# Kernel optimization log

Hardware: AMD Instinct MI355X
Metric: run time of the kernel (lower is better)

## Reference

```python
import jax, jax.numpy as jnp
import numpy as np

B, H, W = 4, 128, 128
D_MODEL = 256
N_LAYERS = 4
N_STATE = 64


def _s4d_kernel(log_dt, logA_re, A_im, C_re, C_im, L):
    """S4D (diagonal SSM) convolution kernel of length L. Shapes: log_dt (d,), others (d,N). Returns (d, L)."""
    dt = jnp.exp(log_dt)                       # (d,)
    A = -jnp.exp(logA_re) + 1j * A_im          # (d,N) complex, Re<0 for stability
    C = C_re + 1j * C_im                       # (d,N)
    dtA = dt[:, None] * A                      # (d,N)
    # ZOH-style input matrix folded into C (S4D-Lin):  C * (exp(dt*A)-1)/A
    CB = C * (jnp.exp(dtA) - 1.0) / A          # (d,N)
    pows = jnp.exp(dtA[:, :, None] * jnp.arange(L, dtype=jnp.float32))  # (d,N,L)
    K = jnp.einsum('dn,dnl->dl', CB, pows)     # (d,L) complex
    return 2.0 * K.real


def _layernorm(x, w, b, eps=1e-5):
    mu = jnp.mean(x, axis=-1, keepdims=True)
    var = jnp.mean(jnp.square(x - mu), axis=-1, keepdims=True)
    return (x - mu) * jax.lax.rsqrt(var + eps) * w + b


def setup_inputs() -> dict:
    key = jax.random.key(0)
    ks = jax.random.split(key, 16)
    d, L, N = D_MODEL, N_LAYERS, N_STATE
    x = jax.random.normal(ks[0], (B, H, W, 1), dtype=jnp.float32)
    grid = jax.random.uniform(ks[1], (B, H, W, 1), dtype=jnp.float32)
    W_enc = jax.random.normal(ks[2], (2, d), dtype=jnp.float32) / np.sqrt(2.0)
    b_enc = jnp.zeros((d,), jnp.float32)
    # per-layer, per-axis (axis 0 = H-kernel, axis 1 = W-kernel) SSM params
    log_dt = jax.random.uniform(ks[3], (L, 2, d), jnp.float32,
                                minval=float(np.log(1e-3)), maxval=float(np.log(1e-1)))
    logA_re = jnp.full((L, 2, d, N), float(np.log(0.5)), jnp.float32)
    A_im = jnp.broadcast_to(np.pi * jnp.arange(N, dtype=jnp.float32), (L, 2, d, N)).copy()
    C_re = jax.random.normal(ks[4], (L, 2, d, N), jnp.float32) * float(0.5 ** 0.5)
    C_im = jax.random.normal(ks[5], (L, 2, d, N), jnp.float32) * float(0.5 ** 0.5)
    Dskip = jax.random.normal(ks[6], (L, d), jnp.float32)
    W_out = jax.random.normal(ks[7], (L, d, 2 * d), jnp.float32) / np.sqrt(d)
    b_out = jnp.zeros((L, 2 * d), jnp.float32)
    ln_w = jnp.ones((L, d), jnp.float32)
    ln_b = jnp.zeros((L, d), jnp.float32)
    W_dec = jax.random.normal(ks[8], (d, 1), jnp.float32) / np.sqrt(d)
    b_dec = jnp.zeros((1,), jnp.float32)
    return dict(x=x, grid=grid, W_enc=W_enc, b_enc=b_enc, log_dt=log_dt,
                logA_re=logA_re, A_im=A_im, C_re=C_re, C_im=C_im, Dskip=Dskip,
                W_out=W_out, b_out=b_out, ln_w=ln_w, ln_b=ln_b, W_dec=W_dec, b_dec=b_dec)


def reference(x, grid, W_enc, b_enc, log_dt, logA_re, A_im, C_re, C_im,
              Dskip, W_out, b_out, ln_w, ln_b, W_dec, b_dec):
    # encoder: concat grid, project to d_model  -> (B,H,W,d)
    h = jnp.concatenate([x, grid], axis=-1) @ W_enc + b_enc
    n_fft = (2 * H, 2 * W)
    for i in range(N_LAYERS):
        z = h
        # separable 2D S4ND kernel: outer product of per-axis S4D kernels
        kh = _s4d_kernel(log_dt[i, 0], logA_re[i, 0], A_im[i, 0], C_re[i, 0], C_im[i, 0], H)  # (d,H)
        kw = _s4d_kernel(log_dt[i, 1], logA_re[i, 1], A_im[i, 1], C_re[i, 1], C_im[i, 1], W)  # (d,W)
        K2 = kh[:, :, None] * kw[:, None, :]                     # (d,H,W)
        u = jnp.transpose(z, (0, 3, 1, 2))                       # (B,d,H,W)
        yf = jnp.fft.rfft2(u, s=n_fft) * jnp.fft.rfft2(K2, s=n_fft)
        y = jnp.fft.irfft2(yf, s=n_fft)[..., :H, :W]             # causal 2D conv via zero-pad FFT
        y = y + u * Dskip[i][:, None, None]                      # skip connection D*u
        y = jnp.transpose(y, (0, 2, 3, 1))                       # back to (B,H,W,d)
        y = jax.nn.gelu(y)
        y = y @ W_out[i] + b_out[i]                              # (B,H,W,2d)
        a, g = jnp.split(y, 2, axis=-1)
        y = a * jax.nn.sigmoid(g)                                # GLU output linear
        h = y + h                                                # residual (dropout=0, eval)
        h = _layernorm(h, ln_w[i], ln_b[i])                      # post-norm (prenorm=False)
    return h @ W_dec + b_dec                                     # (B,H,W,1)
```

## Files before the change

### kernel.cpp

```cpp
#include <hip/hip_runtime.h>
#include <math.h>

#define DM 256
#define NS 64
#define SP 128

typedef __attribute__((ext_vector_type(8))) short bf16x8;
typedef __attribute__((ext_vector_type(4))) float f32x4;

__device__ __forceinline__ float gelu_f(float x) {
    float x3 = x * x * x;
    return 0.5f * x * (1.0f + tanhf(0.7978845608028654f * (x + 0.044715f * x3)));
}
__device__ __forceinline__ float sigmoid_f(float x) {
    return 1.0f / (1.0f + expf(-x));
}
__device__ __forceinline__ unsigned short f2bf(float f) {
    unsigned u = __float_as_uint(f);
    u += 0x7fff + ((u >> 16) & 1);
    return (unsigned short)(u >> 16);
}
__device__ __forceinline__ float bf2f(unsigned short b) {
    return __uint_as_float(((unsigned)b) << 16);
}

__global__ __launch_bounds__(128) void gen_k_kernel(
        const float* __restrict__ log_dt, const float* __restrict__ logA_re,
        const float* __restrict__ A_im,   const float* __restrict__ C_re,
        const float* __restrict__ C_im,   float* __restrict__ Kd) {
    int blk = blockIdx.x;
    int d  = blk & (DM - 1);
    int la = blk >> 8;
    int q  = threadIdx.x;
    __shared__ float s_cbr[NS], s_cbi[NS], s_dr[NS], s_di[NS];
    int pbase = (la * DM + d) * NS;
    float dt = expf(log_dt[la * DM + d]);
    if (q < NS) {
        int n = q;
        float ar = -expf(logA_re[pbase + n]);
        float ai = A_im[pbase + n];
        float dr = dt * ar, di = dt * ai;
        float er = expf(dr);
        float sn, cs;
        sincosf(di, &sn, &cs);
        float nr = er * cs - 1.0f, ni = er * sn;
        float inv = 1.0f / (ar * ar + ai * ai);
        float br = (nr * ar + ni * ai) * inv;
        float bi = (ni * ar - nr * ai) * inv;
        float cr = C_re[pbase + n], ci = C_im[pbase + n];
        s_cbr[n] = cr * br - ci * bi;
        s_cbi[n] = cr * bi + ci * br;
        s_dr[n] = dr;
        s_di[n] = di;
    }
    __syncthreads();
    float fq = (float)q;
    float acc = 0.0f;
    for (int n = 0; n < NS; ++n) {
        float pr = expf(s_dr[n] * fq);
        float sn, cs;
        sincosf(s_di[n] * fq, &sn, &cs);
        acc += s_cbr[n] * (pr * cs) - s_cbi[n] * (pr * sn);
    }
    Kd[((size_t)la * DM + d) * SP + q] = 2.0f * acc;
}

__global__ __launch_bounds__(256) void toep_kernel(
        const float* __restrict__ Kd, unsigned short* __restrict__ Tp, int l) {
    int blk = blockIdx.x;
    int axis = blk >> 8, d = blk & 255;
    int la = l * 2 + axis;
    __shared__ float kt[SP];
    if (threadIdx.x < SP) kt[threadIdx.x] = Kd[((size_t)la * DM + d) * SP + threadIdx.x];
    __syncthreads();
    size_t bse = ((size_t)axis * DM + d) * 16384;
    for (int e = threadIdx.x; e < 16384; e += 256) {
        int i = e >> 7, j = e & 127;
        Tp[bse + e] = (j <= i) ? f2bf(kt[i - j]) : (unsigned short)0;
    }
}

__global__ __launch_bounds__(256) void prep_b_kernel(
        const float* __restrict__ Wo, unsigned short* __restrict__ Bt) {
    int idx = blockIdx.x * 256 + threadIdx.x;
    int l = idx >> 17, rem = idx & 131071, n = rem >> 8, k = rem & 255;
    Bt[idx] = f2bf(Wo[(size_t)l * 131072 + k * 512 + n]);
}

__global__ __launch_bounds__(256) void encode_kernel(
        const float* __restrict__ x, const float* __restrict__ g,
        const float* __restrict__ W_enc, const float* __restrict__ b_enc,
        unsigned short* __restrict__ h) {
    int total = 4 * SP * SP * 128;
    for (int idx = blockIdx.x * blockDim.x + threadIdx.x; idx < total;
         idx += gridDim.x * blockDim.x) {
        int c = (idx & 127) * 2;
        int pos = idx >> 7;
        float xv = x[pos], gv = g[pos];
        float v0 = xv * W_enc[c] + gv * W_enc[DM + c] + b_enc[c];
        float v1 = xv * W_enc[c + 1] + gv * W_enc[DM + c + 1] + b_enc[c + 1];
        unsigned o = (unsigned)f2bf(v0) | ((unsigned)f2bf(v1) << 16);
        *(unsigned*)(h + (size_t)pos * DM + c) = o;
    }
}

template <int FUSE>
__global__ __launch_bounds__(256) void transpose_kernel(
        const unsigned short* __restrict__ in, unsigned short* __restrict__ out,
        int Ci, int Ri, int ctmask, int ctshift,
        const unsigned short* __restrict__ hres, const float* __restrict__ Dsk) {
    __shared__ unsigned tile[64][65];
    int bid = blockIdx.x;
    int rt = bid >> ctshift, ct = bid & ctmask;
    int r0 = rt << 6, c0 = ct << 6;
    int tid = threadIdx.x;
    #pragma unroll
    for (int rep = 0; rep < 2; ++rep) {
        int e = rep * 256 + tid;
        int p = e >> 3, cc = e & 7;
        uint4 v = *(const uint4*)(in + (size_t)(r0 + p) * Ci + c0 + cc * 8);
        const unsigned short* pv = (const unsigned short*)&v;
        #pragma unroll
        for (int q = 0; q < 8; ++q) tile[p][cc * 8 + q] = pv[q];
    }
    __syncthreads();
    #pragma unroll
    for (int rep = 0; rep < 2; ++rep) {
        int e = rep * 256 + tid;
        int cc = e >> 3, pc = e & 7;
        unsigned short tmp[8];
        #pragma unroll
        for (int q = 0; q < 8; ++q) tmp[q] = (unsigned short)tile[pc * 8 + q][cc];
        size_t oaddr = (size_t)(c0 + cc) * Ri + r0 + pc * 8;
        if (FUSE) {
            int d0 = r0 + pc * 8;
            uint4 hv = *(const uint4*)(hres + oaddr);
            const unsigned short* hvp = (const unsigned short*)&hv;
            float4 dk0 = *(const float4*)(Dsk + d0);
            float4 dk1 = *(const float4*)(Dsk + d0 + 4);
            #pragma unroll
            for (int q = 0; q < 8; ++q) {
                float dk = (q < 4) ? (&dk0.x)[q] : (&dk1.x)[q - 4];
                float z = fmaf(bf2f(hvp[q]), dk, bf2f(tmp[q]));
                tmp[q] = f2bf(gelu_f(z));
            }
        }
        *(uint4*)(out + oaddr) = *(const uint4*)tmp;
    }
}

__global__ __launch_bounds__(512, 4) void conv_kernel(
        const unsigned short* __restrict__ hc, const unsigned short* __restrict__ Tp,
        unsigned short* __restrict__ Zc) {
    __shared__ unsigned short Tile[128][128];
    __shared__ unsigned short TpL[128][128];
    int bid = blockIdx.x;
    int work = (bid & 7) * 128 + (bid >> 3);
    int d = work >> 2, b = work & 3;
    int tid = threadIdx.x;
    int lane = tid & 63, wv = tid >> 6;
    int lc = lane & 15, g = lane >> 4;

    const unsigned short* TpW = Tp + (size_t)(DM + d) * 16384;
    const unsigned short* TpH = Tp + (size_t)d * 16384;

    {
        const uint4* srcU = (const uint4*)(hc + ((size_t)d * 4 + b) * 16384);
        const uint4* srcT = (const uint4*)TpW;
        #pragma unroll
        for (int it = 0; it < 4; ++it) {
            int e = it * 512 + tid;
            int r = e >> 4, wc = e & 15;
            *(uint4*)&Tile[r][((wc ^ (r & 7)) << 3)] = srcU[e];
            *(uint4*)&TpL[r][((wc ^ (r & 7)) << 3)] = srcT[e];
        }
    }
    __syncthreads();

    f32x4 acc[8];
    #pragma unroll
    for (int ni = 0; ni < 8; ++ni) acc[ni] = (f32x4){0.f, 0.f, 0.f, 0.f};
    #pragma unroll
    for (int kk = 0; kk < 4; ++kk) {
        int hh = wv * 16 + lc;
        bf16x8 a = *(const bf16x8*)&Tile[hh][(((kk * 4 + g) ^ (hh & 7)) << 3)];
        #pragma unroll
        for (int ni = 0; ni < 8; ++ni) {
            int n = ni * 16 + lc;
            bf16x8 bf = *(const bf16x8*)&TpL[n][(((kk * 4 + g) ^ (n & 7)) << 3)];
            acc[ni] = __builtin_amdgcn_mfma_f32_16x16x32_bf16(a, bf, acc[ni], 0, 0, 0);
        }
    }
    __syncthreads();

    {
        int hh0 = wv * 16 + g * 4;
        #pragma unroll
        for (int ni = 0; ni < 8; ++ni) {
            int w = ni * 16 + lc;
            ushort4 p;
            p.x = f2bf(acc[ni][0]); p.y = f2bf(acc[ni][1]);
            p.z = f2bf(acc[ni][2]); p.w = f2bf(acc[ni][3]);
            *(ushort4*)&Tile[w][((((hh0 >> 3) ^ (w & 7)) << 3) | (hh0 & 7))] = p;
        }
        const uint4* srcT = (const uint4*)TpH;
        #pragma unroll
        for (int it = 0; it < 4; ++it) {
            int e = it * 512 + tid;
            int r = e >> 4, wc = e & 15;
            *(uint4*)&TpL[r][((wc ^ (r & 7)) << 3)] = srcT[e];
        }
    }
    __syncthreads();

    #pragma unroll
    for (int ni = 0; ni < 8; ++ni) acc[ni] = (f32x4){0.f, 0.f, 0.f, 0.f};
    #pragma unroll
    for (int kk = 0; kk < 4; ++kk) {
        int w = wv * 16 + lc;
        bf16x8 a = *(const bf16x8*)&Tile[w][(((kk * 4 + g) ^ (w & 7)) << 3)];
        #pragma unroll
        for (int ni = 0; ni < 8; ++ni) {
            int n = ni * 16 + lc;
            bf16x8 bf = *(const bf16x8*)&TpL[n][(((kk * 4 + g) ^ (n & 7)) << 3)];
            acc[ni] = __builtin_amdgcn_mfma_f32_16x16x32_bf16(a, bf, acc[ni], 0, 0, 0);
        }
    }
    __syncthreads();

    {
        int w0 = wv * 16 + g * 4;
        #pragma unroll
        for (int ni = 0; ni < 8; ++ni) {
            int hh = ni * 16 + lc;
            ushort4 p;
            p.x = f2bf(acc[ni][0]); p.y = f2bf(acc[ni][1]);
            p.z = f2bf(acc[ni][2]); p.w = f2bf(acc[ni][3]);
            *(ushort4*)&Tile[hh][((((w0 >> 3) ^ (hh & 7)) << 3) | (w0 & 7))] = p;
        }
    }
    __syncthreads();
    {
        uint4* dst = (uint4*)(Zc + ((size_t)d * 4 + b) * 16384);
        #pragma unroll
        for (int it = 0; it < 4; ++it) {
            int e = it * 512 + tid;
            int r = e >> 4, wc = e & 15;
            dst[e] = *(const uint4*)&Tile[r][((wc ^ (r & 7)) << 3)];
        }
    }
}

__global__ __launch_bounds__(512, 4) void glu_kernel(
        const unsigned short* __restrict__ Ab, const unsigned short* __restrict__ Bt,
        const unsigned short* __restrict__ h, unsigned short* __restrict__ hp,
        const float* __restrict__ bo) {
    __shared__ unsigned short Ba[64][256];
    __shared__ unsigned short Bg[64][256];
    int tid = threadIdx.x;
    int lane = tid & 63, wv = tid >> 6;
    int lc = lane & 15, g = lane >> 4;
    int m0 = blockIdx.x * 128;
    int mrow = m0 + wv * 16 + lc;

    bf16x8 af[8];
    #pragma unroll
    for (int kk = 0; kk < 8; ++kk)
        af[kk] = *(const bf16x8*)(Ab + (size_t)mrow * DM + kk * 32 + g * 8);

    #pragma unroll
    for (int qp = 0; qp < 4; ++qp) {
        {
            const uint4* srcA = (const uint4*)(Bt + (size_t)(qp * 64) * DM);
            const uint4* srcG = (const uint4*)(Bt + (size_t)(256 + qp * 64) * DM);
            #pragma unroll
            for (int it = 0; it < 4; ++it) {
                int e = it * 512 + tid;
                int r = e >> 5, wc = e & 31;
                *(uint4*)&Ba[r][((wc ^ (r & 7)) << 3)] = srcA[e];
                *(uint4*)&Bg[r][((wc ^ (r & 7)) << 3)] = srcG[e];
            }
        }
        __syncthreads();

        f32x4 aa[4], ag[4];
        #pragma unroll
        for (int ni = 0; ni < 4; ++ni) {
            aa[ni] = (f32x4){0.f, 0.f, 0.f, 0.f};
            ag[ni] = (f32x4){0.f, 0.f, 0.f, 0.f};
        }
        #pragma unroll
        for (int kk = 0; kk < 8; ++kk) {
            #pragma unroll
            for (int ni = 0; ni < 4; ++ni) {
                int r = ni * 16 + lc;
                int ch = (((kk * 4 + g) ^ (r & 7)) << 3);
                bf16x8 bfa = *(const bf16x8*)&Ba[r][ch];
                bf16x8 bfg = *(const bf16x8*)&Bg[r][ch];
                aa[ni] = __builtin_amdgcn_mfma_f32_16x16x32_bf16(bfa, af[kk], aa[ni], 0, 0, 0);
                ag[ni] = __builtin_amdgcn_mfma_f32_16x16x32_bf16(bfg, af[kk], ag[ni], 0, 0, 0);
            }
        }

        #pragma unroll
        for (int ni = 0; ni < 4; ++ni) {
            int ca = qp * 64 + ni * 16 + g * 4;
            float4 bav = *(const float4*)(bo + ca);
            float4 bgv = *(const float4*)(bo + 256 + ca);
            size_t pbase = (size_t)mrow * DM + ca;
            uint2 hv = *(const uint2*)(h + pbase);
            float hr[4];
            hr[0] = __uint_as_float(hv.x << 16);
            hr[1] = __uint_as_float(hv.x & 0xffff0000u);
            hr[2] = __uint_as_float(hv.y << 16);
            hr[3] = __uint_as_float(hv.y & 0xffff0000u);
            float o[4];
            #pragma unroll
            for (int reg = 0; reg < 4; ++reg)
                o[reg] = (aa[ni][reg] + (&bav.x)[reg]) * sigmoid_f(ag[ni][reg] + (&bgv.x)[reg]) + hr[reg];
            uint2 ov;
            ov.x = (unsigned)f2bf(o[0]) | ((unsigned)f2bf(o[1]) << 16);
            ov.y = (unsigned)f2bf(o[2]) | ((unsigned)f2bf(o[3]) << 16);
            *(uint2*)(hp + pbase) = ov;
        }
        __syncthreads();
    }
}

__global__ __launch_bounds__(256) void ln_kernel(
        const unsigned short* __restrict__ hp, unsigned short* __restrict__ h,
        const float* __restrict__ lnw, const float* __restrict__ lnb) {
    int pos = blockIdx.x * 4 + (threadIdx.x >> 6);
    int lane = threadIdx.x & 63;
    size_t base = (size_t)pos * DM + lane * 4;
    uint2 hv = *(const uint2*)(hp + base);
    float v[4];
    v[0] = __uint_as_float(hv.x << 16);
    v[1] = __uint_as_float(hv.x & 0xffff0000u);
    v[2] = __uint_as_float(hv.y << 16);
    v[3] = __uint_as_float(hv.y & 0xffff0000u);
    float s1 = v[0] + v[1] + v[2] + v[3];
    float s2 = v[0] * v[0] + v[1] * v[1] + v[2] * v[2] + v[3] * v[3];
    #pragma unroll
    for (int off = 1; off < 64; off <<= 1) {
        s1 += __shfl_xor(s1, off);
        s2 += __shfl_xor(s2, off);
    }
    float mean = s1 * (1.0f / 256.0f);
    float var = s2 * (1.0f / 256.0f) - mean * mean;
    float inv = rsqrtf(var + 1e-5f);
    float4 w4 = *(const float4*)(lnw + lane * 4);
    float4 b4 = *(const float4*)(lnb + lane * 4);
    float o0 = (v[0] - mean) * inv * w4.x + b4.x;
    float o1 = (v[1] - mean) * inv * w4.y + b4.y;
    float o2 = (v[2] - mean) * inv * w4.z + b4.z;
    float o3 = (v[3] - mean) * inv * w4.w + b4.w;
    uint2 ov;
    ov.x = (unsigned)f2bf(o0) | ((unsigned)f2bf(o1) << 16);
    ov.y = (unsigned)f2bf(o2) | ((unsigned)f2bf(o3) << 16);
    *(uint2*)(h + base) = ov;
}

__global__ __launch_bounds__(256) void decode_kernel(
        const unsigned short* __restrict__ h, const float* __restrict__ Wd,
        const float* __restrict__ bd, float* __restrict__ out) {
    int pos = blockIdx.x * 4 + (threadIdx.x >> 6);
    int lane = threadIdx.x & 63;
    float s = 0.0f;
    #pragma unroll
    for (int j = 0; j < 4; ++j) {
        int d = j * 64 + lane;
        s += bf2f(h[(size_t)pos * DM + d]) * Wd[d];
    }
    #pragma unroll
    for (int off = 32; off > 0; off >>= 1) s += __shfl_down(s, off);
    if (lane == 0) out[pos] = s + bd[0];
}

extern "C" void kernel_launch(void* const* d_in, const int* in_sizes, int n_in,
                              void* d_out, int out_size, void* d_ws, size_t ws_size,
                              hipStream_t stream) {
    const float* x       = (const float*)d_in[0];
    const float* grid    = (const float*)d_in[1];
    const float* W_enc   = (const float*)d_in[2];
    const float* b_enc   = (const float*)d_in[3];
    const float* log_dt  = (const float*)d_in[4];
    const float* logA_re = (const float*)d_in[5];
    const float* A_im    = (const float*)d_in[6];
    const float* C_re    = (const float*)d_in[7];
    const float* C_im    = (const float*)d_in[8];
    const float* Dskip   = (const float*)d_in[9];
    const float* W_out   = (const float*)d_in[10];
    const float* b_out   = (const float*)d_in[11];
    const float* ln_w    = (const float*)d_in[12];
    const float* ln_b    = (const float*)d_in[13];
    const float* W_dec   = (const float*)d_in[14];
    const float* b_dec   = (const float*)d_in[15];

    char* base = (char*)d_ws;
    float*          Kd  = (float*)base;
    unsigned short* Bt  = (unsigned short*)(base + 1048576);
    unsigned short* hP  = (unsigned short*)(base + 2097152);
    unsigned short* R1  = (unsigned short*)(base + 35651584);
    unsigned short* R2  = (unsigned short*)(base + 69206016);
    unsigned short* Tp  = (unsigned short*)(base + 102760448);

    gen_k_kernel<<<dim3(8 * DM), dim3(128), 0, stream>>>(log_dt, logA_re, A_im,
                                                         C_re, C_im, Kd);
    prep_b_kernel<<<dim3(2048), dim3(256), 0, stream>>>(W_out, Bt);
    encode_kernel<<<dim3(2048), dim3(256), 0, stream>>>(x, grid, W_enc, b_enc, hP);

    for (int l = 0; l < 4; ++l) {
        toep_kernel<<<dim3(512), dim3(256), 0, stream>>>(Kd, Tp, l);
        transpose_kernel<0><<<dim3(4096), dim3(256), 0, stream>>>(
            hP, R1, 256, 65536, 3, 2, (const unsigned short*)nullptr, (const float*)nullptr);
        conv_kernel<<<dim3(1024), dim3(512), 0, stream>>>(R1, Tp, R2);
        transpose_kernel<1><<<dim3(4096), dim3(256), 0, stream>>>(
            R2, R1, 65536, 256, 1023, 10, hP, Dskip + (size_t)l * DM);
        glu_kernel<<<dim3(512), dim3(512), 0, stream>>>(R1,
            Bt + (size_t)l * 131072, hP, R2, b_out + (size_t)l * 512);
        ln_kernel<<<dim3(16384), dim3(256), 0, stream>>>(R2, hP,
            ln_w + (size_t)l * DM, ln_b + (size_t)l * DM);
    }

    decode_kernel<<<dim3(16384), dim3(256), 0, stream>>>(hP, W_dec, b_dec,
                                                         (float*)d_out);
}
```

Before: 512.0 us.

## Fuse transposes, skip-GELU, GLU and LayerNorm into one kernel per layer

Replaces the per-layer chain of transpose, transpose+skip+GELU, GLU and LayerNorm kernels with one glu_ln kernel. It reads the channel-major conv output and residual directly, transposes through LDS, and computes GELU, the GEMM with GLU, and the row LayerNorm. It then writes the result in both position-major and channel-major layouts, so the next layer's input transpose is no longer needed. This cuts several full-tensor HBM round trips and launches per layer, at the cost of about 100KB of LDS per block, which lowers occupancy to 2 blocks per CU, plus strided channel-major loads and stores.

Measured after the change: 602.0 us. 1.18x slower.

```diff
diff --git a/kernel.cpp b/kernel.cpp
--- a/kernel.cpp
+++ b/kernel.cpp
@@ -104,11 +104,9 @@
     }
 }
 
-template <int FUSE>
 __global__ __launch_bounds__(256) void transpose_kernel(
         const unsigned short* __restrict__ in, unsigned short* __restrict__ out,
-        int Ci, int Ri, int ctmask, int ctshift,
-        const unsigned short* __restrict__ hres, const float* __restrict__ Dsk) {
+        int Ci, int Ri, int ctmask, int ctshift) {
     __shared__ unsigned tile[64][65];
     int bid = blockIdx.x;
     int rt = bid >> ctshift, ct = bid & ctmask;
@@ -131,21 +129,7 @@
         unsigned short tmp[8];
         #pragma unroll
         for (int q = 0; q < 8; ++q) tmp[q] = (unsigned short)tile[pc * 8 + q][cc];
-        size_t oaddr = (size_t)(c0 + cc) * Ri + r0 + pc * 8;
-        if (FUSE) {
-            int d0 = r0 + pc * 8;
-            uint4 hv = *(const uint4*)(hres + oaddr);
-            const unsigned short* hvp = (const unsigned short*)&hv;
-            float4 dk0 = *(const float4*)(Dsk + d0);
-            float4 dk1 = *(const float4*)(Dsk + d0 + 4);
-            #pragma unroll
-            for (int q = 0; q < 8; ++q) {
-                float dk = (q < 4) ? (&dk0.x)[q] : (&dk1.x)[q - 4];
-                float z = fmaf(bf2f(hvp[q]), dk, bf2f(tmp[q]));
-                tmp[q] = f2bf(gelu_f(z));
-            }
-        }
-        *(uint4*)(out + oaddr) = *(const uint4*)tmp;
+        *(uint4*)(out + (size_t)(c0 + cc) * Ri + r0 + pc * 8) = *(const uint4*)tmp;
     }
 }
 
@@ -251,23 +235,49 @@
     }
 }
 
-__global__ __launch_bounds__(512, 4) void glu_kernel(
-        const unsigned short* __restrict__ Ab, const unsigned short* __restrict__ Bt,
-        const unsigned short* __restrict__ h, unsigned short* __restrict__ hp,
-        const float* __restrict__ bo) {
+__global__ __launch_bounds__(512, 2) void glu_ln_kernel(
+        const unsigned short* __restrict__ Zc, const unsigned short* __restrict__ Bt,
+        unsigned short* __restrict__ hP, unsigned short* __restrict__ hc,
+        const float* __restrict__ Dsk, const float* __restrict__ bo,
+        const float* __restrict__ lnw, const float* __restrict__ lnb) {
     __shared__ unsigned short Ba[64][256];
     __shared__ unsigned short Bg[64][256];
+    __shared__ unsigned short Ot[128][256];
+    __shared__ float rs[128][2];
     int tid = threadIdx.x;
     int lane = tid & 63, wv = tid >> 6;
     int lc = lane & 15, g = lane >> 4;
     int m0 = blockIdx.x * 128;
-    int mrow = m0 + wv * 16 + lc;
+    int arow = wv * 16 + lc;
+    int mrow = m0 + arow;
+
+    #pragma unroll
+    for (int it = 0; it < 8; ++it) {
+        int e = it * 512 + tid;
+        int ch = e >> 4, pck = e & 15;
+        uint4 zv = *(const uint4*)(Zc + (size_t)ch * 65536 + m0 + pck * 8);
+        uint4 hv = *(const uint4*)(hc + (size_t)ch * 65536 + m0 + pck * 8);
+        float dk = Dsk[ch];
+        const unsigned short* zp = (const unsigned short*)&zv;
+        const unsigned short* hq = (const unsigned short*)&hv;
+        #pragma unroll
+        for (int p = 0; p < 8; ++p) {
+            int pos = pck * 8 + p;
+            float a = gelu_f(fmaf(bf2f(hq[p]), dk, bf2f(zp[p])));
+            Ot[pos][(((ch >> 3) ^ (pos & 7)) << 3) | (ch & 7)] = f2bf(a);
+        }
+    }
+    __syncthreads();
 
     bf16x8 af[8];
     #pragma unroll
-    for (int kk = 0; kk < 8; ++kk)
-        af[kk] = *(const bf16x8*)(Ab + (size_t)mrow * DM + kk * 32 + g * 8);
-
+    for (int kk = 0; kk < 8; ++kk) {
+        int ck = (kk * 4 + g) ^ (arow & 7);
+        af[kk] = *(const bf16x8*)&Ot[arow][ck << 3];
+    }
+    __syncthreads();
+
+    float s1 = 0.f, s2 = 0.f;
     #pragma unroll
     for (int qp = 0; qp < 4; ++qp) {
         {
@@ -307,8 +317,7 @@
             int ca = qp * 64 + ni * 16 + g * 4;
             float4 bav = *(const float4*)(bo + ca);
             float4 bgv = *(const float4*)(bo + 256 + ca);
-            size_t pbase = (size_t)mrow * DM + ca;
-            uint2 hv = *(const uint2*)(h + pbase);
+            uint2 hv = *(const uint2*)(hP + (size_t)mrow * DM + ca);
             float hr[4];
             hr[0] = __uint_as_float(hv.x << 16);
             hr[1] = __uint_as_float(hv.x & 0xffff0000u);
@@ -316,49 +325,61 @@
             hr[3] = __uint_as_float(hv.y & 0xffff0000u);
             float o[4];
             #pragma unroll
-            for (int reg = 0; reg < 4; ++reg)
+            for (int reg = 0; reg < 4; ++reg) {
                 o[reg] = (aa[ni][reg] + (&bav.x)[reg]) * sigmoid_f(ag[ni][reg] + (&bgv.x)[reg]) + hr[reg];
-            uint2 ov;
-            ov.x = (unsigned)f2bf(o[0]) | ((unsigned)f2bf(o[1]) << 16);
-            ov.y = (unsigned)f2bf(o[2]) | ((unsigned)f2bf(o[3]) << 16);
-            *(uint2*)(hp + pbase) = ov;
+                s1 += o[reg];
+                s2 += o[reg] * o[reg];
+            }
+            unsigned* wp = (unsigned*)&Ot[arow][((((ca >> 3) ^ (arow & 7)) << 3) | (ca & 7))];
+            wp[0] = (unsigned)f2bf(o[0]) | ((unsigned)f2bf(o[1]) << 16);
+            wp[1] = (unsigned)f2bf(o[2]) | ((unsigned)f2bf(o[3]) << 16);
         }
         __syncthreads();
     }
-}
-
-__global__ __launch_bounds__(256) void ln_kernel(
-        const unsigned short* __restrict__ hp, unsigned short* __restrict__ h,
-        const float* __restrict__ lnw, const float* __restrict__ lnb) {
-    int pos = blockIdx.x * 4 + (threadIdx.x >> 6);
-    int lane = threadIdx.x & 63;
-    size_t base = (size_t)pos * DM + lane * 4;
-    uint2 hv = *(const uint2*)(hp + base);
-    float v[4];
-    v[0] = __uint_as_float(hv.x << 16);
-    v[1] = __uint_as_float(hv.x & 0xffff0000u);
-    v[2] = __uint_as_float(hv.y << 16);
-    v[3] = __uint_as_float(hv.y & 0xffff0000u);
-    float s1 = v[0] + v[1] + v[2] + v[3];
-    float s2 = v[0] * v[0] + v[1] * v[1] + v[2] * v[2] + v[3] * v[3];
-    #pragma unroll
-    for (int off = 1; off < 64; off <<= 1) {
-        s1 += __shfl_xor(s1, off);
-        s2 += __shfl_xor(s2, off);
-    }
+
+    s1 += __shfl_xor(s1, 16); s2 += __shfl_xor(s2, 16);
+    s1 += __shfl_xor(s1, 32); s2 += __shfl_xor(s2, 32);
     float mean = s1 * (1.0f / 256.0f);
     float var = s2 * (1.0f / 256.0f) - mean * mean;
     float inv = rsqrtf(var + 1e-5f);
-    float4 w4 = *(const float4*)(lnw + lane * 4);
-    float4 b4 = *(const float4*)(lnb + lane * 4);
-    float o0 = (v[0] - mean) * inv * w4.x + b4.x;
-    float o1 = (v[1] - mean) * inv * w4.y + b4.y;
-    float o2 = (v[2] - mean) * inv * w4.z + b4.z;
-    float o3 = (v[3] - mean) * inv * w4.w + b4.w;
-    uint2 ov;
-    ov.x = (unsigned)f2bf(o0) | ((unsigned)f2bf(o1) << 16);
-    ov.y = (unsigned)f2bf(o2) | ((unsigned)f2bf(o3) << 16);
-    *(uint2*)(h + base) = ov;
+    if (g == 0) { rs[arow][0] = mean; rs[arow][1] = inv; }
+    __syncthreads();
+
+    #pragma unroll
+    for (int it = 0; it < 8; ++it) {
+        int e = it * 512 + tid;
+        int row = e >> 5, ck = e & 31;
+        int c0 = ck * 8;
+        uint4 v = *(const uint4*)&Ot[row][((ck ^ (row & 7)) << 3)];
+        const unsigned short* vp = (const unsigned short*)&v;
+        float mn = rs[row][0], iv = rs[row][1];
+        float4 w0 = *(const float4*)(lnw + c0);
+        float4 w1 = *(const float4*)(lnw + c0 + 4);
+        float4 b0 = *(const float4*)(lnb + c0);
+        float4 b1 = *(const float4*)(lnb + c0 + 4);
+        unsigned short tmp[8];
+        #pragma unroll
+        for (int q = 0; q < 8; ++q) {
+            float lw = (q < 4) ? (&w0.x)[q] : (&w1.x)[q - 4];
+            float lb = (q < 4) ? (&b0.x)[q] : (&b1.x)[q - 4];
+            tmp[q] = f2bf((bf2f(vp[q]) - mn) * iv * lw + lb);
+        }
+        *(uint4*)(hP + (size_t)(m0 + row) * DM + c0) = *(const uint4*)tmp;
+    }
+    #pragma unroll
+    for (int it = 0; it < 8; ++it) {
+        int e = it * 512 + tid;
+        int ch = e >> 4, pck = e & 15;
+        float lw = lnw[ch], lb = lnb[ch];
+        unsigned short tmp[8];
+        #pragma unroll
+        for (int p = 0; p < 8; ++p) {
+            int pos = pck * 8 + p;
+            float v = bf2f(Ot[pos][(((ch >> 3) ^ (pos & 7)) << 3) | (ch & 7)]);
+            tmp[p] = f2bf((v - rs[pos][0]) * rs[pos][1] * lw + lb);
+        }
+        *(uint4*)(hc + (size_t)ch * 65536 + m0 + pck * 8) = *(const uint4*)tmp;
+    }
 }
 
 __global__ __launch_bounds__(256) void decode_kernel(
@@ -401,25 +422,22 @@
     float*          Kd  = (float*)base;
     unsigned short* Bt  = (unsigned short*)(base + 1048576);
     unsigned short* hP  = (unsigned short*)(base + 2097152);
-    unsigned short* R1  = (unsigned short*)(base + 35651584);
-    unsigned short* R2  = (unsigned short*)(base + 69206016);
+    unsigned short* HC  = (unsigned short*)(base + 35651584);
+    unsigned short* ZC  = (unsigned short*)(base + 69206016);
     unsigned short* Tp  = (unsigned short*)(base + 102760448);
 
     gen_k_kernel<<<dim3(8 * DM), dim3(128), 0, stream>>>(log_dt, logA_re, A_im,
                                                          C_re, C_im, Kd);
     prep_b_kernel<<<dim3(2048), dim3(256), 0, stream>>>(W_out, Bt);
     encode_kernel<<<dim3(2048), dim3(256), 0, stream>>>(x, grid, W_enc, b_enc, hP);
+    transpose_kernel<<<dim3(4096), dim3(256), 0, stream>>>(hP, HC, 256, 65536, 3, 2);
 
     for (int l = 0; l < 4; ++l) {
         toep_kernel<<<dim3(512), dim3(256), 0, stream>>>(Kd, Tp, l);
-        transpose_kernel<0><<<dim3(4096), dim3(256), 0, stream>>>(
-            hP, R1, 256, 65536, 3, 2, (const unsigned short*)nullptr, (const float*)nullptr);
-        conv_kernel<<<dim3(1024), dim3(512), 0, stream>>>(R1, Tp, R2);
-        transpose_kernel<1><<<dim3(4096), dim3(256), 0, stream>>>(
-            R2, R1, 65536, 256, 1023, 10, hP, Dskip + (size_t)l * DM);
-        glu_kernel<<<dim3(512), dim3(512), 0, stream>>>(R1,
-            Bt + (size_t)l * 131072, hP, R2, b_out + (size_t)l * 512);
-        ln_kernel<<<dim3(16384), dim3(256), 0, stream>>>(R2, hP,
+        conv_kernel<<<dim3(1024), dim3(512), 0, stream>>>(HC, Tp, ZC);
+        glu_ln_kernel<<<dim3(512), dim3(512), 0, stream>>>(ZC,
+            Bt + (size_t)l * 131072, hP, HC,
+            Dskip + (size_t)l * DM, b_out + (size_t)l * 512,
             ln_w + (size_t)l * DM, ln_b + (size_t)l * DM);
     }
 
```

## Fuse layernorm with channel-major transpose and restructure GLU tiling per output quarter

Applied to the files above, without the earlier changes.

The per-layer channel-major transpose moves into a new layernorm kernel. That kernel normalizes rows in place and also writes the transposed copy that the next layer's conv reads, so one full pass over the activations per layer is removed. Only the initial transpose stays outside the loop. The GLU kernel is restructured so each block loads one 64-column slice of the weights once and reuses it across 512 rows. It now writes its output in place into h instead of into a separate buffer. The risk is an in-place hazard: GLU reads h as the residual and writes h in the same place, which is fine only while each element is read before it is written by the same thread.

Result: slower. 533.3 us (+4.2%).

```diff
diff --git a/kernel.cpp b/kernel.cpp
--- a/kernel.cpp
+++ b/kernel.cpp
@@ -253,35 +253,35 @@
 
 __global__ __launch_bounds__(512, 4) void glu_kernel(
         const unsigned short* __restrict__ Ab, const unsigned short* __restrict__ Bt,
-        const unsigned short* __restrict__ h, unsigned short* __restrict__ hp,
-        const float* __restrict__ bo) {
+        unsigned short* __restrict__ h, const float* __restrict__ bo) {
     __shared__ unsigned short Ba[64][256];
     __shared__ unsigned short Bg[64][256];
     int tid = threadIdx.x;
     int lane = tid & 63, wv = tid >> 6;
     int lc = lane & 15, g = lane >> 4;
-    int m0 = blockIdx.x * 128;
-    int mrow = m0 + wv * 16 + lc;
-
-    bf16x8 af[8];
-    #pragma unroll
-    for (int kk = 0; kk < 8; ++kk)
-        af[kk] = *(const bf16x8*)(Ab + (size_t)mrow * DM + kk * 32 + g * 8);
-
-    #pragma unroll
-    for (int qp = 0; qp < 4; ++qp) {
-        {
-            const uint4* srcA = (const uint4*)(Bt + (size_t)(qp * 64) * DM);
-            const uint4* srcG = (const uint4*)(Bt + (size_t)(256 + qp * 64) * DM);
-            #pragma unroll
-            for (int it = 0; it < 4; ++it) {
-                int e = it * 512 + tid;
-                int r = e >> 5, wc = e & 31;
-                *(uint4*)&Ba[r][((wc ^ (r & 7)) << 3)] = srcA[e];
-                *(uint4*)&Bg[r][((wc ^ (r & 7)) << 3)] = srcG[e];
-            }
-        }
-        __syncthreads();
+    int mb = blockIdx.x & 127;
+    int qp = blockIdx.x >> 7;
+
+    {
+        const uint4* srcA = (const uint4*)(Bt + (size_t)(qp * 64) * DM);
+        const uint4* srcG = (const uint4*)(Bt + (size_t)(256 + qp * 64) * DM);
+        #pragma unroll
+        for (int it = 0; it < 4; ++it) {
+            int e = it * 512 + tid;
+            int r = e >> 5, wc = e & 31;
+            *(uint4*)&Ba[r][((wc ^ (r & 7)) << 3)] = srcA[e];
+            *(uint4*)&Bg[r][((wc ^ (r & 7)) << 3)] = srcG[e];
+        }
+    }
+    __syncthreads();
+
+    #pragma unroll
+    for (int s4 = 0; s4 < 4; ++s4) {
+        int mrow = mb * 512 + s4 * 128 + wv * 16 + lc;
+        bf16x8 af[8];
+        #pragma unroll
+        for (int kk = 0; kk < 8; ++kk)
+            af[kk] = *(const bf16x8*)(Ab + (size_t)mrow * DM + kk * 32 + g * 8);
 
         f32x4 aa[4], ag[4];
         #pragma unroll
@@ -321,44 +321,82 @@
             uint2 ov;
             ov.x = (unsigned)f2bf(o[0]) | ((unsigned)f2bf(o[1]) << 16);
             ov.y = (unsigned)f2bf(o[2]) | ((unsigned)f2bf(o[3]) << 16);
-            *(uint2*)(hp + pbase) = ov;
+            *(uint2*)(h + pbase) = ov;
+        }
+    }
+}
+
+__global__ __launch_bounds__(256) void ln_tr_kernel(
+        unsigned short* __restrict__ hio, unsigned short* __restrict__ hc,
+        const float* __restrict__ lnw, const float* __restrict__ lnb) {
+    __shared__ unsigned tile[64][65];
+    __shared__ float rs[64][2];
+    int r0 = blockIdx.x * 64;
+    int tid = threadIdx.x;
+    int wv = tid >> 6, lane = tid & 63;
+
+    for (int it = 0; it < 16; ++it) {
+        int p = it * 4 + wv;
+        size_t base = (size_t)(r0 + p) * DM + lane * 4;
+        uint2 hv = *(const uint2*)(hio + base);
+        float v0 = __uint_as_float(hv.x << 16);
+        float v1 = __uint_as_float(hv.x & 0xffff0000u);
+        float v2 = __uint_as_float(hv.y << 16);
+        float v3 = __uint_as_float(hv.y & 0xffff0000u);
+        float s1 = v0 + v1 + v2 + v3;
+        float s2 = v0 * v0 + v1 * v1 + v2 * v2 + v3 * v3;
+        #pragma unroll
+        for (int off = 1; off < 64; off <<= 1) {
+            s1 += __shfl_xor(s1, off);
+            s2 += __shfl_xor(s2, off);
+        }
+        if (lane == 0) {
+            float mean = s1 * (1.0f / 256.0f);
+            float var = s2 * (1.0f / 256.0f) - mean * mean;
+            rs[p][0] = mean;
+            rs[p][1] = rsqrtf(var + 1e-5f);
+        }
+    }
+    __syncthreads();
+
+    for (int ct = 0; ct < 4; ++ct) {
+        int c0 = ct * 64;
+        #pragma unroll
+        for (int rep = 0; rep < 2; ++rep) {
+            int e = rep * 256 + tid;
+            int p = e >> 3, cc = e & 7;
+            size_t addr = (size_t)(r0 + p) * DM + c0 + cc * 8;
+            uint4 v = *(const uint4*)(hio + addr);
+            const unsigned short* vp = (const unsigned short*)&v;
+            float mn = rs[p][0], iv = rs[p][1];
+            int cb = c0 + cc * 8;
+            float4 w0 = *(const float4*)(lnw + cb);
+            float4 w1 = *(const float4*)(lnw + cb + 4);
+            float4 b0 = *(const float4*)(lnb + cb);
+            float4 b1 = *(const float4*)(lnb + cb + 4);
+            unsigned short tmp[8];
+            #pragma unroll
+            for (int q = 0; q < 8; ++q) {
+                float lw = (q < 4) ? (&w0.x)[q] : (&w1.x)[q - 4];
+                float lb = (q < 4) ? (&b0.x)[q] : (&b1.x)[q - 4];
+                tmp[q] = f2bf((bf2f(vp[q]) - mn) * iv * lw + lb);
+            }
+            *(uint4*)(hio + addr) = *(const uint4*)tmp;
+            #pragma unroll
+            for (int q = 0; q < 8; ++q) tile[p][cc * 8 + q] = tmp[q];
         }
         __syncthreads();
-    }
-}
-
-__global__ __launch_bounds__(256) void ln_kernel(
-        const unsigned short* __restrict__ hp, unsigned short* __restrict__ h,
-        const float* __restrict__ lnw, const float* __restrict__ lnb) {
-    int pos = blockIdx.x * 4 + (threadIdx.x >> 6);
-    int lane = threadIdx.x & 63;
-    size_t base = (size_t)pos * DM + lane * 4;
-    uint2 hv = *(const uint2*)(hp + base);
-    float v[4];
-    v[0] = __uint_as_float(hv.x << 16);
-    v[1] = __uint_as_float(hv.x & 0xffff0000u);
-    v[2] = __uint_as_float(hv.y << 16);
-    v[3] = __uint_as_float(hv.y & 0xffff0000u);
-    float s1 = v[0] + v[1] + v[2] + v[3];
-    float s2 = v[0] * v[0] + v[1] * v[1] + v[2] * v[2] + v[3] * v[3];
-    #pragma unroll
-    for (int off = 1; off < 64; off <<= 1) {
-        s1 += __shfl_xor(s1, off);
-        s2 += __shfl_xor(s2, off);
-    }
-    float mean = s1 * (1.0f / 256.0f);
-    float var = s2 * (1.0f / 256.0f) - mean * mean;
-    float inv = rsqrtf(var + 1e-5f);
-    float4 w4 = *(const float4*)(lnw + lane * 4);
-    float4 b4 = *(const float4*)(lnb + lane * 4);
-    float o0 = (v[0] - mean) * inv * w4.x + b4.x;
-    float o1 = (v[1] - mean) * inv * w4.y + b4.y;
-    float o2 = (v[2] - mean) * inv * w4.z + b4.z;
-    float o3 = (v[3] - mean) * inv * w4.w + b4.w;
-    uint2 ov;
-    ov.x = (unsigned)f2bf(o0) | ((unsigned)f2bf(o1) << 16);
-    ov.y = (unsigned)f2bf(o2) | ((unsigned)f2bf(o3) << 16);
-    *(uint2*)(h + base) = ov;
+        #pragma unroll
+        for (int rep = 0; rep < 2; ++rep) {
+            int e = rep * 256 + tid;
+            int cc = e >> 3, pc = e & 7;
+            unsigned short tmp[8];
+            #pragma unroll
+            for (int q = 0; q < 8; ++q) tmp[q] = (unsigned short)tile[pc * 8 + q][cc];
+            *(uint4*)(hc + (size_t)(c0 + cc) * 65536 + r0 + pc * 8) = *(const uint4*)tmp;
+        }
+        __syncthreads();
+    }
 }
 
 __global__ __launch_bounds__(256) void decode_kernel(
@@ -409,17 +447,17 @@
                                                          C_re, C_im, Kd);
     prep_b_kernel<<<dim3(2048), dim3(256), 0, stream>>>(W_out, Bt);
     encode_kernel<<<dim3(2048), dim3(256), 0, stream>>>(x, grid, W_enc, b_enc, hP);
+    transpose_kernel<0><<<dim3(4096), dim3(256), 0, stream>>>(
+        hP, R1, 256, 65536, 3, 2, (const unsigned short*)nullptr, (const float*)nullptr);
 
     for (int l = 0; l < 4; ++l) {
         toep_kernel<<<dim3(512), dim3(256), 0, stream>>>(Kd, Tp, l);
-        transpose_kernel<0><<<dim3(4096), dim3(256), 0, stream>>>(
-            hP, R1, 256, 65536, 3, 2, (const unsigned short*)nullptr, (const float*)nullptr);
         conv_kernel<<<dim3(1024), dim3(512), 0, stream>>>(R1, Tp, R2);
         transpose_kernel<1><<<dim3(4096), dim3(256), 0, stream>>>(
             R2, R1, 65536, 256, 1023, 10, hP, Dskip + (size_t)l * DM);
         glu_kernel<<<dim3(512), dim3(512), 0, stream>>>(R1,
-            Bt + (size_t)l * 131072, hP, R2, b_out + (size_t)l * 512);
-        ln_kernel<<<dim3(16384), dim3(256), 0, stream>>>(R2, hP,
+            Bt + (size_t)l * 131072, hP, b_out + (size_t)l * 512);
+        ln_tr_kernel<<<dim3(1024), dim3(256), 0, stream>>>(hP, R1,
             ln_w + (size_t)l * DM, ln_b + (size_t)l * DM);
     }
 
```
